# Kernel optimization log

Measured on AMD Instinct MI355X. Metric: run time of the kernel, lower is better.

The kernel has to match this reference:

```python
import jax, jax.numpy as jnp
import numpy as np

N_NODES = 100000
N_EDGES = 3200000
D_IN = 128
D_OUT = 128


def setup_inputs() -> dict:
    key = jax.random.key(0)
    k1, k2, k3, k4, k5 = jax.random.split(key, 5)
    x = jax.random.normal(k1, (N_NODES, D_IN), dtype=jnp.float32)
    adj_rows = jax.random.randint(k2, (N_EDGES,), 0, N_NODES, dtype=jnp.int64)
    adj_cols = jax.random.randint(k3, (N_EDGES,), 0, N_NODES, dtype=jnp.int64)
    adj_vals = jax.random.uniform(k4, (N_EDGES,), dtype=jnp.float32)
    # torch Linear weight has shape (dim_out, dim_in)
    W = jax.random.normal(k5, (D_OUT, D_IN), dtype=jnp.float32) * (1.0 / np.sqrt(D_IN))
    return {"x": x, "adj_rows": adj_rows, "adj_cols": adj_cols, "adj_vals": adj_vals, "W": W}


def reference(x, adj_rows, adj_cols, adj_vals, W):
    # h = Linear(x) with no bias: x @ W^T  -> [N, D_OUT]
    h = x @ W.T
    # sparse.mm(adjacency, h): out[r] = sum_e vals[e] * h[cols[e]] for edges with rows[e]==r
    msgs = adj_vals[:, None] * h[adj_cols]           # [E, D_OUT]
    agg = jax.ops.segment_sum(msgs, adj_rows, num_segments=N_NODES)
    return jax.nn.relu(agg)
```

## Files before the change

kernel.cpp:

```cpp
#include <hip/hip_runtime.h>
#include <stdint.h>

typedef unsigned short u16;
typedef unsigned int u32;
typedef unsigned long long u64;
typedef __attribute__((ext_vector_type(8))) short short8;
typedef __attribute__((ext_vector_type(4))) float floatx4;

#define DIM 128
#define DIM2 64
#define NBK 1792
#define NBK_PT 7
#define NB_SH 6
#define AGG_NB 64
#define AGG_CAP 2560
#define SC_C 8192

__device__ __forceinline__ u32 f32_to_bf16_rne(float f) {
  u32 u = __float_as_uint(f);
  u32 r = u + 0x7fffu + ((u >> 16) & 1u);
  return r >> 16;
}
__device__ __forceinline__ float bf16_to_f32(u32 u) { return __uint_as_float(u << 16); }
__device__ __forceinline__ u32 pack2bf16(float a, float b) {
  return f32_to_bf16_rne(a) | (f32_to_bf16_rne(b) << 16);
}

union FragU {
  u32 d[4];
  short8 s;
};

__global__ __launch_bounds__(256) void gemm_mfma(const float* __restrict__ x,
                                                 const float* __restrict__ W,
                                                 u16* __restrict__ h, int N) {
  __shared__ u32 Wl[DIM * DIM2];
  int tid = threadIdx.x;
#pragma unroll
  for (int i = 0; i < 8; ++i) {
    int ga = tid + 256 * i;
    int o = ga >> 4, g = ga & 15;
    const float* src = W + (size_t)o * DIM + g * 8;
    floatx4 f0 = *(const floatx4*)src;
    floatx4 f1 = *(const floatx4*)(src + 4);
    int slot = (g + o) & 15;
    u32* dst = &Wl[o * DIM2 + slot * 4];
    dst[0] = pack2bf16(f0.x, f0.y);
    dst[1] = pack2bf16(f0.z, f0.w);
    dst[2] = pack2bf16(f1.x, f1.y);
    dst[3] = pack2bf16(f1.z, f1.w);
  }
  __syncthreads();

  int lane = tid & 63;
  int wave = tid >> 6;
  int m = lane & 15;
  int kg = lane >> 4;
  int ntile = (N + 63) >> 6;

  for (int t = blockIdx.x; t < ntile; t += 256) {
    int nodeBase = t * 64 + wave * 16;
    if (nodeBase >= N) continue;

    short8 a[4];
    const float* xr = x + (size_t)(nodeBase + m) * DIM + kg * 8;
#pragma unroll
    for (int kt = 0; kt < 4; ++kt) {
      floatx4 f0 = *(const floatx4*)(xr + kt * 32);
      floatx4 f1 = *(const floatx4*)(xr + kt * 32 + 4);
      FragU fu;
      fu.d[0] = pack2bf16(f0.x, f0.y);
      fu.d[1] = pack2bf16(f0.z, f0.w);
      fu.d[2] = pack2bf16(f1.x, f1.y);
      fu.d[3] = pack2bf16(f1.z, f1.w);
      a[kt] = fu.s;
    }

#pragma unroll
    for (int ot = 0; ot < 8; ++ot) {
      int o = ot * 16 + m;
      floatx4 acc = {0.f, 0.f, 0.f, 0.f};
#pragma unroll
      for (int kt = 0; kt < 4; ++kt) {
        int slot = (kt * 4 + kg + o) & 15;
        short8 b = *(short8*)&Wl[o * DIM2 + slot * 4];
        acc = __builtin_amdgcn_mfma_f32_16x16x32_bf16(a[kt], b, acc, 0, 0, 0);
      }
#pragma unroll
      for (int r = 0; r < 4; ++r) {
        int node = nodeBase + kg * 4 + r;
        h[(size_t)node * DIM + ot * 16 + m] = (u16)f32_to_bf16_rne(acc[r]);
      }
    }
  }
}

__device__ __forceinline__ void scan_nbk(u32* cnt, u32* excl, u32* wtot) {
  int tid = threadIdx.x, lane = tid & 63, wave = tid >> 6;
  u32 c[NBK_PT], sum = 0;
#pragma unroll
  for (int k = 0; k < NBK_PT; ++k) {
    c[k] = cnt[tid * NBK_PT + k];
    sum += c[k];
  }
  u32 inc = sum;
#pragma unroll
  for (int d = 1; d < 64; d <<= 1) {
    u32 t = __shfl_up(inc, d, 64);
    if (lane >= d) inc += t;
  }
  if (lane == 63) wtot[wave] = inc;
  __syncthreads();
  u32 wbase = 0;
  for (int w = 0; w < wave; ++w) wbase += wtot[w];
  u32 run = wbase + inc - sum;
#pragma unroll
  for (int k = 0; k < NBK_PT; ++k) {
    excl[tid * NBK_PT + k] = run;
    run += c[k];
  }
  __syncthreads();
}

__global__ __launch_bounds__(256) void sort_scatter(const int* __restrict__ rows,
                                                    const int* __restrict__ cols,
                                                    const float* __restrict__ vals,
                                                    u32* __restrict__ bcol,
                                                    u16* __restrict__ bval,
                                                    u32* __restrict__ dir, int E, int B) {
  __shared__ u32 hist[NBK];
  __shared__ u32 starts[NBK];
  __shared__ u32 wtot[4];
  __shared__ u32 s_lo[SC_C];
  __shared__ u16 s_val[SC_C];
  int tid = threadIdx.x;
  int wg = blockIdx.x;
  int base = wg * SC_C;
  int tot = min(SC_C, E - base);

  for (int b = tid; b < NBK; b += 256) hist[b] = 0;
  __syncthreads();
  for (int j = tid; j < tot; j += 256) {
    atomicAdd(&hist[((u32)rows[base + j]) >> NB_SH], 1u);
  }
  __syncthreads();
  scan_nbk(hist, starts, wtot);
  for (int b = tid; b < NBK; b += 256) hist[b] = starts[b];
  __syncthreads();
  for (int j = tid; j < tot; j += 256) {
    u32 r = (u32)rows[base + j];
    u32 bk = r >> NB_SH;
    u32 p = atomicAdd(&hist[bk], 1u);
    s_lo[p] = ((r & 63u) << 26) | ((u32)cols[base + j] << 8);
    s_val[p] = (u16)f32_to_bf16_rne(vals[base + j]);
  }
  __syncthreads();
  for (int i = tid; i < tot; i += 256) {
    bcol[(size_t)base + i] = s_lo[i];
    bval[(size_t)base + i] = s_val[i];
  }
  for (int b = tid; b < B; b += 256) {
    dir[(size_t)wg * B + b] = (starts[b] << 16) | (hist[b] - starts[b]);
  }
}

__global__ __launch_bounds__(256) void agg_bucket(const u32* __restrict__ bcol,
                                                  const u16* __restrict__ bval,
                                                  const u32* __restrict__ dir,
                                                  const u32* __restrict__ h,
                                                  float* __restrict__ out, int N,
                                                  int nsc, int B) {
  __shared__ u64 s_rec[AGG_CAP];
  __shared__ u32 segdir[512], segdst[512];
  __shared__ u32 cnt[AGG_NB], excl[AGG_NB], ptr[AGG_NB], wtot[4];
  int tid = threadIdx.x, lane = tid & 63, wave = tid >> 6;
  int b = blockIdx.x;
  int nodeBase = b << NB_SH;
  int lane4 = lane * 4;
  const char* hb = (const char*)h;

  for (int w = tid; w < nsc; w += 256) segdir[w] = dir[(size_t)w * B + b];
  if (tid < AGG_NB) cnt[tid] = 0;
  __syncthreads();
  {
    int e0 = 2 * tid, e1 = e0 + 1;
    u32 c0 = (e0 < nsc) ? (segdir[e0] & 0xffffu) : 0u;
    u32 c1 = (e1 < nsc) ? (segdir[e1] & 0xffffu) : 0u;
    u32 s = c0 + c1, inc = s;
#pragma unroll
    for (int d = 1; d < 64; d <<= 1) {
      u32 t = __shfl_up(inc, d, 64);
      if (lane >= d) inc += t;
    }
    if (lane == 63) wtot[wave] = inc;
    __syncthreads();
    u32 wbase = 0;
    for (int w = 0; w < wave; ++w) wbase += wtot[w];
    u32 ex = wbase + inc - s;
    segdst[e0] = ex;
    segdst[e1] = ex + c0;
    __syncthreads();
  }
  int T = (int)(wtot[0] + wtot[1] + wtot[2] + wtot[3]);

  if (T <= AGG_CAP) {
    u32 rlo[10], rv[10];
#pragma unroll
    for (int k = 0; k < 10; ++k) {
      int g = tid + 256 * k;
      rlo[k] = 0;
      rv[k] = 0;
      if (g < T) {
        int lo = 0, hi = nsc - 1;
        while (lo < hi) {
          int mid = (lo + hi + 1) >> 1;
          if (segdst[mid] <= (u32)g) lo = mid; else hi = mid - 1;
        }
        u32 dv = segdir[lo];
        u32 src = (u32)lo * SC_C + (dv >> 16) + ((u32)g - segdst[lo]);
        rlo[k] = bcol[src];
        rv[k] = bval[src];
        atomicAdd(&cnt[rlo[k] >> 26], 1u);
      }
    }
    __syncthreads();
    if (tid < 64) {
      u32 c = cnt[tid], inc = c;
#pragma unroll
      for (int d = 1; d < 64; d <<= 1) {
        u32 t = __shfl_up(inc, d, 64);
        if (lane >= d) inc += t;
      }
      excl[tid] = inc - c;
      ptr[tid] = inc - c;
    }
    __syncthreads();
#pragma unroll
    for (int k = 0; k < 10; ++k) {
      int g = tid + 256 * k;
      if (g < T) {
        u32 p = atomicAdd(&ptr[rlo[k] >> 26], 1u);
        s_rec[p] = ((u64)(rv[k] << 16) << 32) | rlo[k];
      }
    }
    __syncthreads();
    int wbeg = (int)excl[wave * 16];
    int wend = (int)ptr[wave * 16 + 15];
    float a0 = 0.f, a1 = 0.f;
    int curn = -1;
    for (int e = wbeg; e < wend; e += 8) {
      u32 lo8[8];
      float v8[8];
      u32 hd[8];
#pragma unroll
      for (int g = 0; g < 8; ++g) {
        int ee = e + g;
        bool act = ee < wend;
        u64 r = s_rec[act ? ee : (wend - 1)];
        lo8[g] = (u32)r;
        v8[g] = act ? __uint_as_float((u32)(r >> 32)) : 0.f;
      }
#pragma unroll
      for (int g = 0; g < 8; ++g) {
        hd[g] = *(const u32*)(hb + ((lo8[g] & 0x01FFFF00u) + lane4));
      }
#pragma unroll
      for (int g = 0; g < 8; ++g) {
        int nid = __builtin_amdgcn_readfirstlane((int)(lo8[g] >> 26));
        if (nid != curn) {
          if (curn >= 0) {
            float2 o = make_float2(fmaxf(a0, 0.f), fmaxf(a1, 0.f));
            *(float2*)(out + (size_t)(nodeBase + curn) * DIM + 2 * lane) = o;
          }
          curn = nid;
          a0 = 0.f;
          a1 = 0.f;
        }
        float v = v8[g];
        a0 += v * bf16_to_f32(hd[g] & 0xffffu);
        a1 += v * bf16_to_f32(hd[g] >> 16);
      }
    }
    if (curn >= 0) {
      float2 o = make_float2(fmaxf(a0, 0.f), fmaxf(a1, 0.f));
      *(float2*)(out + (size_t)(nodeBase + curn) * DIM + 2 * lane) = o;
    }
    for (int nn = 0; nn < 16; ++nn) {
      int nl = wave * 16 + nn;
      int node = nodeBase + nl;
      if (cnt[nl] == 0 && node < N) {
        *(float2*)(out + (size_t)node * DIM + 2 * lane) = make_float2(0.f, 0.f);
      }
    }
  } else {
    for (int nn = 0; nn < 16; ++nn) {
      int nl = wave * 16 + nn;
      int node = nodeBase + nl;
      if (node >= N) continue;
      float a0 = 0.f, a1 = 0.f;
      for (int w = 0; w < nsc; ++w) {
        u32 dv = segdir[w];
        int sc = (int)(dv & 0xffffu);
        u32 so = dv >> 16;
        for (int r = 0; r < sc; ++r) {
          u32 lo = bcol[(size_t)w * SC_C + so + r];
          if ((int)(lo >> 26) == nl) {
            u32 d = *(const u32*)(hb + ((lo & 0x01FFFF00u) + lane4));
            float v = bf16_to_f32(bval[(size_t)w * SC_C + so + r]);
            a0 += v * bf16_to_f32(d & 0xffffu);
            a1 += v * bf16_to_f32(d >> 16);
          }
        }
      }
      *(float2*)(out + (size_t)node * DIM + 2 * lane) =
          make_float2(fmaxf(a0, 0.f), fmaxf(a1, 0.f));
    }
  }
}

extern "C" void kernel_launch(void* const* d_in, const int* in_sizes, int n_in,
                              void* d_out, int out_size, void* d_ws, size_t ws_size,
                              hipStream_t stream) {
  const float* x    = (const float*)d_in[0];
  const int*   rows = (const int*)d_in[1];
  const int*   cols = (const int*)d_in[2];
  const float* vals = (const float*)d_in[3];
  const float* W    = (const float*)d_in[4];

  const int N = in_sizes[0] / DIM;
  const int E = in_sizes[1];
  const int B = (N + AGG_NB - 1) / AGG_NB;
  const int nsc = (E + SC_C - 1) / SC_C;

  char* wsb = (char*)d_ws;
  size_t o = 0;
  u16* h = (u16*)wsb;            o += (size_t)N * DIM * sizeof(u16);
  u32* bcol = (u32*)(wsb + o);   o += (size_t)nsc * SC_C * sizeof(u32);
  u16* bval = (u16*)(wsb + o);   o += (size_t)nsc * SC_C * sizeof(u16);
  u32* dir  = (u32*)(wsb + o);   o += (size_t)nsc * B * sizeof(u32);

  gemm_mfma<<<256, 256, 0, stream>>>(x, W, h, N);
  sort_scatter<<<nsc, 256, 0, stream>>>(rows, cols, vals, bcol, bval, dir, E, B);
  agg_bucket<<<B, 256, 0, stream>>>(bcol, bval, dir, (const u32*)h,
                                    (float*)d_out, N, nsc, B);
}
```

Before: 342.7 us.

## Double aggregation bucket width to 128 nodes and transpose bucket directory

Widens each aggregation bucket from 64 to 128 destination nodes, which halves the bucket count to 782 and shrinks the sort histogram to 1024 entries. Each agg block now holds up to 4608 edge records in shared memory and keeps 18 records per thread in registers, with 32 nodes per wave. The segment directory is stored transposed, so each agg block reads its per-chunk entries contiguously instead of with a stride. The trade-off is fewer, heavier blocks with more LDS and register use, which lowers occupancy, and a larger share of blocks may take the slow fallback path when a bucket overflows its capacity.

After: 394.5 us. 15.1% more time.

```diff
diff --git a/kernel.cpp b/kernel.cpp
--- a/kernel.cpp
+++ b/kernel.cpp
@@ -9,12 +9,12 @@
 
 #define DIM 128
 #define DIM2 64
-#define NBK 1792
-#define NBK_PT 7
-#define NB_SH 6
-#define AGG_NB 64
-#define AGG_CAP 2560
+#define NBK 1024
+#define NB_SH 7
+#define AGG_NB 128
+#define AGG_CAP 4608
 #define SC_C 8192
+#define NSEG 512
 
 __device__ __forceinline__ u32 f32_to_bf16_rne(float f) {
   u32 u = __float_as_uint(f);
@@ -95,12 +95,12 @@
   }
 }
 
-__device__ __forceinline__ void scan_nbk(u32* cnt, u32* excl, u32* wtot) {
+__device__ __forceinline__ void scan1024(u32* cnt, u32* excl, u32* wtot) {
   int tid = threadIdx.x, lane = tid & 63, wave = tid >> 6;
-  u32 c[NBK_PT], sum = 0;
-#pragma unroll
-  for (int k = 0; k < NBK_PT; ++k) {
-    c[k] = cnt[tid * NBK_PT + k];
+  u32 c[4], sum = 0;
+#pragma unroll
+  for (int k = 0; k < 4; ++k) {
+    c[k] = cnt[tid * 4 + k];
     sum += c[k];
   }
   u32 inc = sum;
@@ -115,8 +115,8 @@
   for (int w = 0; w < wave; ++w) wbase += wtot[w];
   u32 run = wbase + inc - sum;
 #pragma unroll
-  for (int k = 0; k < NBK_PT; ++k) {
-    excl[tid * NBK_PT + k] = run;
+  for (int k = 0; k < 4; ++k) {
+    excl[tid * 4 + k] = run;
     run += c[k];
   }
   __syncthreads();
@@ -127,7 +127,8 @@
                                                     const float* __restrict__ vals,
                                                     u32* __restrict__ bcol,
                                                     u16* __restrict__ bval,
-                                                    u32* __restrict__ dir, int E, int B) {
+                                                    u32* __restrict__ dirT, int E, int B,
+                                                    int nsc) {
   __shared__ u32 hist[NBK];
   __shared__ u32 starts[NBK];
   __shared__ u32 wtot[4];
@@ -144,14 +145,14 @@
     atomicAdd(&hist[((u32)rows[base + j]) >> NB_SH], 1u);
   }
   __syncthreads();
-  scan_nbk(hist, starts, wtot);
+  scan1024(hist, starts, wtot);
   for (int b = tid; b < NBK; b += 256) hist[b] = starts[b];
   __syncthreads();
   for (int j = tid; j < tot; j += 256) {
     u32 r = (u32)rows[base + j];
     u32 bk = r >> NB_SH;
     u32 p = atomicAdd(&hist[bk], 1u);
-    s_lo[p] = ((r & 63u) << 26) | ((u32)cols[base + j] << 8);
+    s_lo[p] = ((r & 127u) << 25) | ((u32)cols[base + j] << 8);
     s_val[p] = (u16)f32_to_bf16_rne(vals[base + j]);
   }
   __syncthreads();
@@ -160,18 +161,18 @@
     bval[(size_t)base + i] = s_val[i];
   }
   for (int b = tid; b < B; b += 256) {
-    dir[(size_t)wg * B + b] = (starts[b] << 16) | (hist[b] - starts[b]);
+    dirT[(size_t)b * nsc + wg] = (starts[b] << 16) | (hist[b] - starts[b]);
   }
 }
 
 __global__ __launch_bounds__(256) void agg_bucket(const u32* __restrict__ bcol,
                                                   const u16* __restrict__ bval,
-                                                  const u32* __restrict__ dir,
+                                                  const u32* __restrict__ dirT,
                                                   const u32* __restrict__ h,
                                                   float* __restrict__ out, int N,
                                                   int nsc, int B) {
   __shared__ u64 s_rec[AGG_CAP];
-  __shared__ u32 segdir[512], segdst[512];
+  __shared__ u32 segdir[NSEG], segdst[NSEG];
   __shared__ u32 cnt[AGG_NB], excl[AGG_NB], ptr[AGG_NB], wtot[4];
   int tid = threadIdx.x, lane = tid & 63, wave = tid >> 6;
   int b = blockIdx.x;
@@ -179,7 +180,7 @@
   int lane4 = lane * 4;
   const char* hb = (const char*)h;
 
-  for (int w = tid; w < nsc; w += 256) segdir[w] = dir[(size_t)w * B + b];
+  for (int w = tid; w < nsc; w += 256) segdir[w] = dirT[(size_t)b * nsc + w];
   if (tid < AGG_NB) cnt[tid] = 0;
   __syncthreads();
   {
@@ -204,9 +205,9 @@
   int T = (int)(wtot[0] + wtot[1] + wtot[2] + wtot[3]);
 
   if (T <= AGG_CAP) {
-    u32 rlo[10], rv[10];
-#pragma unroll
-    for (int k = 0; k < 10; ++k) {
+    u32 rlo[18], rv[18];
+#pragma unroll
+    for (int k = 0; k < 18; ++k) {
       int g = tid + 256 * k;
       rlo[k] = 0;
       rv[k] = 0;
@@ -220,32 +221,36 @@
         u32 src = (u32)lo * SC_C + (dv >> 16) + ((u32)g - segdst[lo]);
         rlo[k] = bcol[src];
         rv[k] = bval[src];
-        atomicAdd(&cnt[rlo[k] >> 26], 1u);
+        atomicAdd(&cnt[rlo[k] >> 25], 1u);
       }
     }
     __syncthreads();
     if (tid < 64) {
-      u32 c = cnt[tid], inc = c;
+      u32 c0 = cnt[2 * lane], c1 = cnt[2 * lane + 1];
+      u32 s = c0 + c1, inc = s;
 #pragma unroll
       for (int d = 1; d < 64; d <<= 1) {
         u32 t = __shfl_up(inc, d, 64);
         if (lane >= d) inc += t;
       }
-      excl[tid] = inc - c;
-      ptr[tid] = inc - c;
-    }
-    __syncthreads();
-#pragma unroll
-    for (int k = 0; k < 10; ++k) {
+      u32 ex = inc - s;
+      excl[2 * lane] = ex;
+      ptr[2 * lane] = ex;
+      excl[2 * lane + 1] = ex + c0;
+      ptr[2 * lane + 1] = ex + c0;
+    }
+    __syncthreads();
+#pragma unroll
+    for (int k = 0; k < 18; ++k) {
       int g = tid + 256 * k;
       if (g < T) {
-        u32 p = atomicAdd(&ptr[rlo[k] >> 26], 1u);
+        u32 p = atomicAdd(&ptr[rlo[k] >> 25], 1u);
         s_rec[p] = ((u64)(rv[k] << 16) << 32) | rlo[k];
       }
     }
     __syncthreads();
-    int wbeg = (int)excl[wave * 16];
-    int wend = (int)ptr[wave * 16 + 15];
+    int wbeg = (int)excl[wave * 32];
+    int wend = (int)ptr[wave * 32 + 31];
     float a0 = 0.f, a1 = 0.f;
     int curn = -1;
     for (int e = wbeg; e < wend; e += 8) {
@@ -266,7 +271,7 @@
       }
 #pragma unroll
       for (int g = 0; g < 8; ++g) {
-        int nid = __builtin_amdgcn_readfirstlane((int)(lo8[g] >> 26));
+        int nid = __builtin_amdgcn_readfirstlane((int)(lo8[g] >> 25));
         if (nid != curn) {
           if (curn >= 0) {
             float2 o = make_float2(fmaxf(a0, 0.f), fmaxf(a1, 0.f));
@@ -285,16 +290,16 @@
       float2 o = make_float2(fmaxf(a0, 0.f), fmaxf(a1, 0.f));
       *(float2*)(out + (size_t)(nodeBase + curn) * DIM + 2 * lane) = o;
     }
-    for (int nn = 0; nn < 16; ++nn) {
-      int nl = wave * 16 + nn;
+    for (int nn = 0; nn < 32; ++nn) {
+      int nl = wave * 32 + nn;
       int node = nodeBase + nl;
       if (cnt[nl] == 0 && node < N) {
         *(float2*)(out + (size_t)node * DIM + 2 * lane) = make_float2(0.f, 0.f);
       }
     }
   } else {
-    for (int nn = 0; nn < 16; ++nn) {
-      int nl = wave * 16 + nn;
+    for (int nn = 0; nn < 32; ++nn) {
+      int nl = wave * 32 + nn;
       int node = nodeBase + nl;
       if (node >= N) continue;
       float a0 = 0.f, a1 = 0.f;
@@ -304,7 +309,7 @@
         u32 so = dv >> 16;
         for (int r = 0; r < sc; ++r) {
           u32 lo = bcol[(size_t)w * SC_C + so + r];
-          if ((int)(lo >> 26) == nl) {
+          if ((int)(lo >> 25) == nl) {
             u32 d = *(const u32*)(hb + ((lo & 0x01FFFF00u) + lane4));
             float v = bf16_to_f32(bval[(size_t)w * SC_C + so + r]);
             a0 += v * bf16_to_f32(d & 0xffffu);
@@ -337,10 +342,10 @@
   u16* h = (u16*)wsb;            o += (size_t)N * DIM * sizeof(u16);
   u32* bcol = (u32*)(wsb + o);   o += (size_t)nsc * SC_C * sizeof(u32);
   u16* bval = (u16*)(wsb + o);   o += (size_t)nsc * SC_C * sizeof(u16);
-  u32* dir  = (u32*)(wsb + o);   o += (size_t)nsc * B * sizeof(u32);
+  u32* dirT = (u32*)(wsb + o);   o += (size_t)B * nsc * sizeof(u32);
 
   gemm_mfma<<<256, 256, 0, stream>>>(x, W, h, N);
-  sort_scatter<<<nsc, 256, 0, stream>>>(rows, cols, vals, bcol, bval, dir, E, B);
-  agg_bucket<<<B, 256, 0, stream>>>(bcol, bval, dir, (const u32*)h,
+  sort_scatter<<<nsc, 256, 0, stream>>>(rows, cols, vals, bcol, bval, dirT, E, B, nsc);
+  agg_bucket<<<B, 256, 0, stream>>>(bcol, bval, dirT, (const u32*)h,
                                     (float*)d_out, N, nsc, B);
 }
```

## Transpose bucket directory, enlarge sort chunks, replace binary search with LDS map

Applied to the files above, without the earlier changes.

Sort chunk size grows from 8192 to 12800 edges, which cuts the number of segments to 250 (under a fixed cap of 256). The per-chunk bucket directory is stored transposed so each aggregation block reads its segment entries contiguously instead of with a large stride. The per-edge binary search over segment offsets is replaced by an LDS map from edge slot to segment id, built by serial per-segment fill loops. Larger chunks raise shared-memory use in sort_scatter and lower its block count. The map fill is serial per segment, and the fixed 256-segment cap and 16-bit packed offsets limit scalability.

New measurement: 345.4 us. About the same (+0.8%).

```diff
diff --git a/kernel.cpp b/kernel.cpp
--- a/kernel.cpp
+++ b/kernel.cpp
@@ -14,7 +14,8 @@
 #define NB_SH 6
 #define AGG_NB 64
 #define AGG_CAP 2560
-#define SC_C 8192
+#define SC_C 12800
+#define NSEG 256
 
 __device__ __forceinline__ u32 f32_to_bf16_rne(float f) {
   u32 u = __float_as_uint(f);
@@ -127,7 +128,8 @@
                                                     const float* __restrict__ vals,
                                                     u32* __restrict__ bcol,
                                                     u16* __restrict__ bval,
-                                                    u32* __restrict__ dir, int E, int B) {
+                                                    u32* __restrict__ dirT, int E, int B,
+                                                    int nsc) {
   __shared__ u32 hist[NBK];
   __shared__ u32 starts[NBK];
   __shared__ u32 wtot[4];
@@ -160,50 +162,63 @@
     bval[(size_t)base + i] = s_val[i];
   }
   for (int b = tid; b < B; b += 256) {
-    dir[(size_t)wg * B + b] = (starts[b] << 16) | (hist[b] - starts[b]);
+    dirT[(size_t)b * nsc + wg] = (starts[b] << 16) | (hist[b] - starts[b]);
   }
 }
 
 __global__ __launch_bounds__(256) void agg_bucket(const u32* __restrict__ bcol,
                                                   const u16* __restrict__ bval,
-                                                  const u32* __restrict__ dir,
+                                                  const u32* __restrict__ dirT,
                                                   const u32* __restrict__ h,
                                                   float* __restrict__ out, int N,
                                                   int nsc, int B) {
   __shared__ u64 s_rec[AGG_CAP];
-  __shared__ u32 segdir[512], segdst[512];
-  __shared__ u32 cnt[AGG_NB], excl[AGG_NB], ptr[AGG_NB], wtot[4];
+  __shared__ u16 map[AGG_CAP];
+  __shared__ u32 segdir[NSEG], segdst[NSEG];
+  __shared__ u32 cnt[AGG_NB], excl[AGG_NB], ptr[AGG_NB];
+  __shared__ u32 sT;
   int tid = threadIdx.x, lane = tid & 63, wave = tid >> 6;
   int b = blockIdx.x;
   int nodeBase = b << NB_SH;
   int lane4 = lane * 4;
   const char* hb = (const char*)h;
 
-  for (int w = tid; w < nsc; w += 256) segdir[w] = dir[(size_t)w * B + b];
+  for (int w = tid; w < NSEG; w += 256)
+    segdir[w] = (w < nsc) ? dirT[(size_t)b * nsc + w] : 0u;
   if (tid < AGG_NB) cnt[tid] = 0;
   __syncthreads();
-  {
-    int e0 = 2 * tid, e1 = e0 + 1;
-    u32 c0 = (e0 < nsc) ? (segdir[e0] & 0xffffu) : 0u;
-    u32 c1 = (e1 < nsc) ? (segdir[e1] & 0xffffu) : 0u;
-    u32 s = c0 + c1, inc = s;
+  if (tid < 64) {
+    u32 c[4], sum = 0;
+#pragma unroll
+    for (int k = 0; k < 4; ++k) {
+      c[k] = segdir[lane * 4 + k] & 0xffffu;
+      sum += c[k];
+    }
+    u32 inc = sum;
 #pragma unroll
     for (int d = 1; d < 64; d <<= 1) {
       u32 t = __shfl_up(inc, d, 64);
       if (lane >= d) inc += t;
     }
-    if (lane == 63) wtot[wave] = inc;
+    u32 run = inc - sum;
+#pragma unroll
+    for (int k = 0; k < 4; ++k) {
+      segdst[lane * 4 + k] = run;
+      run += c[k];
+    }
+    if (lane == 63) sT = inc;
+  }
+  __syncthreads();
+  int T = (int)sT;
+
+  if (T <= AGG_CAP) {
+    for (int w = tid; w < nsc; w += 256) {
+      u32 dv = segdir[w];
+      u32 c = dv & 0xffffu;
+      u32 d0 = segdst[w];
+      for (u32 i = 0; i < c; ++i) map[d0 + i] = (u16)w;
+    }
     __syncthreads();
-    u32 wbase = 0;
-    for (int w = 0; w < wave; ++w) wbase += wtot[w];
-    u32 ex = wbase + inc - s;
-    segdst[e0] = ex;
-    segdst[e1] = ex + c0;
-    __syncthreads();
-  }
-  int T = (int)(wtot[0] + wtot[1] + wtot[2] + wtot[3]);
-
-  if (T <= AGG_CAP) {
     u32 rlo[10], rv[10];
 #pragma unroll
     for (int k = 0; k < 10; ++k) {
@@ -211,13 +226,9 @@
       rlo[k] = 0;
       rv[k] = 0;
       if (g < T) {
-        int lo = 0, hi = nsc - 1;
-        while (lo < hi) {
-          int mid = (lo + hi + 1) >> 1;
-          if (segdst[mid] <= (u32)g) lo = mid; else hi = mid - 1;
-        }
-        u32 dv = segdir[lo];
-        u32 src = (u32)lo * SC_C + (dv >> 16) + ((u32)g - segdst[lo]);
+        int w = map[g];
+        u32 dv = segdir[w];
+        u32 src = (u32)w * SC_C + (dv >> 16) + ((u32)g - segdst[w]);
         rlo[k] = bcol[src];
         rv[k] = bval[src];
         atomicAdd(&cnt[rlo[k] >> 26], 1u);
@@ -337,10 +348,10 @@
   u16* h = (u16*)wsb;            o += (size_t)N * DIM * sizeof(u16);
   u32* bcol = (u32*)(wsb + o);   o += (size_t)nsc * SC_C * sizeof(u32);
   u16* bval = (u16*)(wsb + o);   o += (size_t)nsc * SC_C * sizeof(u16);
-  u32* dir  = (u32*)(wsb + o);   o += (size_t)nsc * B * sizeof(u32);
+  u32* dirT = (u32*)(wsb + o);   o += (size_t)B * nsc * sizeof(u32);
 
   gemm_mfma<<<256, 256, 0, stream>>>(x, W, h, N);
-  sort_scatter<<<nsc, 256, 0, stream>>>(rows, cols, vals, bcol, bval, dir, E, B);
-  agg_bucket<<<B, 256, 0, stream>>>(bcol, bval, dir, (const u32*)h,
+  sort_scatter<<<nsc, 256, 0, stream>>>(rows, cols, vals, bcol, bval, dirT, E, B, nsc);
+  agg_bucket<<<B, 256, 0, stream>>>(bcol, bval, dirT, (const u32*)h,
                                     (float*)d_out, N, nsc, B);
 }
```
